# Performance work log

Hardware: AMD Instinct MI355X
Metric: run time of the kernel (lower is better)

Reference implementation:

```python
import jax, jax.numpy as jnp
import numpy as np

UNITS = 50257
CUTOFF = [2000, 10000, UNITS]  # _cutoff = cutoff + [units]
C = 1024                        # channels (d_model)
N = 4096                        # flattened tokens (batch*seq)
N_TAILS = len(CUTOFF) - 1       # 2
ROOT_OUT = CUTOFF[0] + N_TAILS  # 2002
TAIL_DIMS = [256, 64]           # round(C/4**(i+1)/8)*8


def setup_inputs() -> dict:
    key = jax.random.key(0)
    ks = jax.random.split(key, 7)
    logits = jax.random.normal(ks[0], (N, C), jnp.float32)
    targets = jax.random.randint(ks[1], (N,), 0, UNITS, jnp.int32)
    s = 0.02
    head_kernel = jax.random.normal(ks[2], (C, ROOT_OUT), jnp.float32) * s
    proj0 = jax.random.normal(ks[3], (C, TAIL_DIMS[0]), jnp.float32) * s
    scale0 = jax.random.normal(ks[4], (TAIL_DIMS[0], CUTOFF[1] - CUTOFF[0]), jnp.float32) * s
    proj1 = jax.random.normal(ks[5], (C, TAIL_DIMS[1]), jnp.float32) * s
    scale1 = jax.random.normal(ks[6], (TAIL_DIMS[1], CUTOFF[2] - CUTOFF[1]), jnp.float32) * s
    return {"logits": logits, "targets": targets, "head_kernel": head_kernel,
            "proj0": proj0, "scale0": scale0, "proj1": proj1, "scale1": scale1}


def _sparse_ce(lg, labels):
    # sparse softmax cross entropy, numerically stable (single logsumexp)
    lse = jax.nn.logsumexp(lg, axis=-1)
    picked = jnp.take_along_axis(lg, labels[:, None].astype(jnp.int32), axis=1)[:, 0]
    return lse - picked


def reference(logits, targets, head_kernel, proj0, scale0, proj1, scale1):
    # Faithful jax version of AdaptiveSoftmax._train_loss (return_probs=False,
    # dropout=0, no bias on Denses, loss_reduction=SUM_OVER_BATCH_SIZE i.e. mean).
    # Dynamic boolean gather is replaced by dense compute + masked mean, which
    # yields identical math under jit (mean over the routed subset).
    root_logits = (logits @ head_kernel).astype(jnp.float32)  # [N, ROOT_OUT]
    root_targets = targets
    tails = [(proj0, scale0), (proj1, scale1)]
    losses = []
    for i, (p, s) in enumerate(tails):
        lo, hi = CUTOFF[i], CUTOFF[i + 1]
        m = (targets >= lo) & (targets < hi)
        root_targets = jnp.where(m, CUTOFF[0] + i, root_targets)
        tail_logits = ((logits @ p) @ s).astype(jnp.float32)  # [N, hi-lo]
        tail_tgt = jnp.clip(targets - lo, 0, hi - lo - 1)
        ce = _sparse_ce(tail_logits, tail_tgt)
        mf = m.astype(jnp.float32)
        losses.append(jnp.sum(ce * mf) / jnp.maximum(jnp.sum(mf), 1.0))
    root_loss = jnp.mean(_sparse_ce(root_logits, root_targets))
    all_losses = jnp.stack([root_loss] + losses)
    return jnp.mean(all_losses)
```

## Files before the change

### kernel.cpp

```cpp
#include <hip/hip_runtime.h>
#include <math.h>
#include <stdint.h>

#define NROWS 4096
#define CDIM 1024
#define T0_LO 2000
#define T0_HI 10000
#define T1_LO 10000
#define ROOT_COLS 2002
#define ROOT_PAD 2048
#define T0_COLS 8000
#define T0_PAD 8064
#define T1_COLS 40257
#define T1_PAD 40320
#define HB_STRIDE 320
#define LOG2E 1.44269504088896340736f
#define LN2 0.69314718055994530942f

using short8  = __attribute__((ext_vector_type(8))) short;
using ushort8 = __attribute__((ext_vector_type(8))) unsigned short;
using floatx4 = __attribute__((ext_vector_type(4))) float;

__device__ __forceinline__ unsigned short f2bf(float x) {
  union { float f; unsigned int u; } v; v.f = x;
  unsigned int r = v.u + 0x7fffu + ((v.u >> 16) & 1u);
  return (unsigned short)(r >> 16);
}
__device__ __forceinline__ float bf2f(unsigned short h) {
  union { unsigned int u; float f; } v; v.u = ((unsigned int)h) << 16;
  return v.f;
}
__device__ __forceinline__ floatx4 mfma16(short8 a, short8 b, floatx4 c) {
  return __builtin_amdgcn_mfma_f32_16x16x32_bf16(a, b, c, 0, 0, 0);
}
__device__ __forceinline__ void stage16(const unsigned short* g,
                                        unsigned short* lds_wave_base, int lane) {
#if __has_builtin(__builtin_amdgcn_global_load_lds)
  __builtin_amdgcn_global_load_lds(
      (const __attribute__((address_space(1))) void*)g,
      (__attribute__((address_space(3))) void*)lds_wave_base, 16, 0, 0);
#else
  ((ushort8*)lds_wave_base)[lane] = *(const ushort8*)g;
#endif
}

static constexpr size_t B_HB  = 0;
static constexpr size_t B_LB  = B_HB + 4096ull * 320 * 2;
static constexpr size_t B_WP  = B_LB + 4096ull * 1024 * 2;
static constexpr size_t B_WH  = B_WP + 384ull * 1024 * 2;
static constexpr size_t B_WS0 = B_WH + 2048ull * 1024 * 2;
static constexpr size_t B_WS1 = B_WS0 + 8064ull * 256 * 2;
static constexpr size_t B_S   = B_WS1 + 40320ull * 64 * 2;
static constexpr size_t B_P   = B_S + 3ull * 4096 * 4;
static constexpr size_t B_I0  = B_P + 3ull * 4096 * 4;
static constexpr size_t B_I1  = B_I0 + 4096ull * 4;
static constexpr size_t B_CNT = B_I1 + 4096ull * 4;

__device__ __forceinline__ void transpose_tile(
    const float* __restrict__ W, unsigned short* __restrict__ Wt,
    int K, int N, int Npad, int nx, int rel, float scale,
    float (*tile)[33], int tid) {
  const int n0 = (rel % nx) * 32, k0 = (rel / nx) * 32;
  if ((N & 3) == 0) {
    const int lk = tid >> 3, ln = (tid & 7) << 2;
    const int n = n0 + ln;
    float4 v = make_float4(0.f, 0.f, 0.f, 0.f);
    if (n + 3 < N) v = *(const float4*)(W + (size_t)(k0 + lk) * N + n);
    tile[lk][ln]     = v.x * scale;
    tile[lk][ln + 1] = v.y * scale;
    tile[lk][ln + 2] = v.z * scale;
    tile[lk][ln + 3] = v.w * scale;
  } else if ((N & 1) == 0) {
    const int lk = tid >> 4, ln = (tid & 15) << 1;
#pragma unroll
    for (int i = 0; i < 32; i += 16) {
      const int n = n0 + ln;
      float2 v = make_float2(0.f, 0.f);
      if (n + 1 < N) v = *(const float2*)(W + (size_t)(k0 + lk + i) * N + n);
      tile[lk + i][ln]     = v.x * scale;
      tile[lk + i][ln + 1] = v.y * scale;
    }
  } else {
    const int tx = tid & 31, ty = tid >> 5;
    for (int i = 0; i < 32; i += 8) {
      int k = k0 + ty + i, n = n0 + tx;
      tile[ty + i][tx] = (n < N) ? W[(size_t)k * N + n] * scale : 0.f;
    }
  }
  __syncthreads();
  if (tid < 128) {
    const int nloc = tid >> 2, kg = tid & 3;
    const int n = n0 + nloc;
    if (n < Npad) {
      ushort8 x;
#pragma unroll
      for (int j = 0; j < 8; j++) x[j] = f2bf(tile[kg * 8 + j][nloc]);
      *(ushort8*)&Wt[(size_t)n * K + k0 + kg * 8] = x;
    }
  }
}

#define PP_WH_END   2048
#define PP_WS0_END  (PP_WH_END + 2016)
#define PP_WS1_END  (PP_WS0_END + 2520)
#define PP_WP0_END  (PP_WS1_END + 256)
#define PP_WP1_END  (PP_WP0_END + 64)
#define PP_LB_END   (PP_WP1_END + 2048)
#define PP_ZERO_END (PP_LB_END + 32)
#define PP_S_END    (PP_ZERO_END + 4)
#define PP_TOTAL    (PP_S_END + 1)

__global__ __launch_bounds__(256) void prep_kernel(
    const float* __restrict__ head, const float* __restrict__ proj0,
    const float* __restrict__ proj1, const float* __restrict__ scale0,
    const float* __restrict__ scale1, const float* __restrict__ logits,
    const int* __restrict__ targets,
    unsigned short* __restrict__ Wh, unsigned short* __restrict__ Wp,
    unsigned short* __restrict__ Ws0, unsigned short* __restrict__ Ws1,
    unsigned short* __restrict__ Lb, float* __restrict__ S,
    int* __restrict__ idx0, int* __restrict__ idx1, int* __restrict__ cnt) {
  __shared__ float tile[32][33];
  const int id = blockIdx.x, tid = threadIdx.x;
  if (id < PP_WP1_END) {
    const float* W; unsigned short* Wt; int K, N, Npad, nx, rel; float scale;
    if (id < PP_WH_END)        { W = head;   Wt = Wh;  K = 1024; N = ROOT_COLS; Npad = ROOT_PAD; scale = LOG2E; nx = 64;   rel = id; }
    else if (id < PP_WS0_END)  { W = scale0; Wt = Ws0; K = 256;  N = T0_COLS;   Npad = T0_PAD;   scale = LOG2E; nx = 252;  rel = id - PP_WH_END; }
    else if (id < PP_WS1_END)  { W = scale1; Wt = Ws1; K = 64;   N = T1_COLS;   Npad = T1_PAD;   scale = LOG2E; nx = 1260; rel = id - PP_WS0_END; }
    else if (id < PP_WP0_END)  { W = proj0;  Wt = Wp;  K = 1024; N = 256;       Npad = 256;      scale = 1.f;   nx = 8;    rel = id - PP_WS1_END; }
    else                       { W = proj1;  Wt = Wp + 256 * 1024; K = 1024; N = 64; Npad = 64; scale = 1.f; nx = 2; rel = id - PP_WP0_END; }
    transpose_tile(W, Wt, K, N, Npad, nx, rel, scale, tile, tid);
    return;
  }
  if (id < PP_LB_END) {
    size_t base = (size_t)(id - PP_WP1_END) * 2048 + tid * 8;
    float4 v0 = *(const float4*)(logits + base);
    float4 v1 = *(const float4*)(logits + base + 4);
    ushort8 h;
    h[0] = f2bf(v0.x); h[1] = f2bf(v0.y); h[2] = f2bf(v0.z); h[3] = f2bf(v0.w);
    h[4] = f2bf(v1.x); h[5] = f2bf(v1.y); h[6] = f2bf(v1.z); h[7] = f2bf(v1.w);
    *(ushort8*)(Lb + base) = h;
    return;
  }
  if (id < PP_ZERO_END) {
    size_t off = (size_t)(id - PP_LB_END) * 2048 + tid * 8;
    ushort8 z = {0, 0, 0, 0, 0, 0, 0, 0};
    *(ushort8*)(Wp + 320ull * 1024 + off) = z;
    return;
  }
  if (id < PP_S_END) {
    int rel = id - PP_ZERO_END;
    float4 z = make_float4(0.f, 0.f, 0.f, 0.f);
#pragma unroll
    for (int j = 0; j < 3; j++)
      ((float4*)S)[rel * 768 + j * 256 + tid] = z;
    return;
  }
  __shared__ int base2[2];
  if (tid < 2) base2[tid] = 0;
  __syncthreads();
  for (int n = tid; n < NROWS; n += 256) {
    int t = targets[n];
    if (t >= T0_LO && t < T0_HI) idx0[atomicAdd(&base2[0], 1)] = n;
    else if (t >= T1_LO)         idx1[atomicAdd(&base2[1], 1)] = n;
  }
  __syncthreads();
  if (tid < 2) cnt[tid] = base2[tid];
}

template<int CI>
__device__ __forceinline__ void gemm64_kloop(
    unsigned short* A_lds,
    const unsigned short* Arow,
    const unsigned short* const (&Bbase)[CI],
    floatx4 (&acc)[CI][4], int tid) {
  const int lane = tid & 63, w = tid >> 6;
  const int m = lane & 15, quad = lane >> 4, keym = m & 7;
  int goff[4];
#pragma unroll
  for (int it = 0; it < 4; it++) {
    int s = w * 256 + it * 64 + lane;
    int r = s >> 4, p = s & 15;
    int cq = p ^ (r & 7);
    goff[it] = r * CDIM + cq * 8;
  }
#pragma unroll
  for (int it = 0; it < 4; it++)
    stage16(Arow + goff[it], &A_lds[(w * 256 + it * 64) * 8], lane);
  for (int h = 0; h < 8; h++) {
    unsigned short* cur = A_lds + (h & 1) * (64 * 128);
    unsigned short* nxt = A_lds + ((h + 1) & 1) * (64 * 128);
    __syncthreads();
    if (h + 1 < 8) {
#pragma unroll
      for (int it = 0; it < 4; it++)
        stage16(Arow + goff[it] + (h + 1) * 128,
                &nxt[(w * 256 + it * 64) * 8], lane);
    }
    short8 b[CI][4];
#pragma unroll
    for (int ci = 0; ci < CI; ci++)
#pragma unroll
      for (int ks = 0; ks < 4; ks++)
        b[ci][ks] = *(const short8*)(Bbase[ci] + h * 128 + ks * 32);
    short8 areg[4][4];
#pragma unroll
    for (int t = 0; t < 4; t++)
#pragma unroll
      for (int ks = 0; ks < 4; ks++) {
        int ch = ((ks << 2) + quad) ^ keym;
        areg[t][ks] = *(const short8*)&cur[(t * 16 + m) * 128 + (ch << 3)];
      }
#pragma unroll
    for (int ci = 0; ci < CI; ci++)
#pragma unroll
      for (int ks = 0; ks < 4; ks++)
#pragma unroll
        for (int t = 0; t < 4; t++)
          acc[ci][t] = mfma16(areg[t][ks], b[ci][ks], acc[ci][t]);
  }
}

__global__ __launch_bounds__(256) void hidden_kernel(
    const unsigned short* __restrict__ Lb,
    const unsigned short* __restrict__ Wp,
    unsigned short* __restrict__ Hb) {
  __shared__ unsigned short A_lds[64 * 256];
  const int id = blockIdx.x, tid = threadIdx.x;
  const int xcd = id & 7, k = id >> 3;
  const int row0 = (xcd * 8 + (k & 7)) * 64;
  const int cg0 = k >> 3;
  const int lane = tid & 63, w = tid >> 6;
  const int m = lane & 15, quad = lane >> 4;
  const floatx4 zf = {0.f, 0.f, 0.f, 0.f};
  floatx4 acc[1][4];
#pragma unroll
  for (int t = 0; t < 4; t++) acc[0][t] = zf;
  const unsigned short* Bb[1] = {
      Wp + (size_t)(cg0 * 64 + w * 16 + m) * CDIM + quad * 8};
  gemm64_kloop<1>(A_lds, Lb + (size_t)row0 * CDIM, Bb, acc, tid);
  int n = cg0 * 64 + w * 16 + m;
  if (n < HB_STRIDE) {
#pragma unroll
    for (int t = 0; t < 4; t++)
#pragma unroll
      for (int r = 0; r < 4; r++)
        Hb[(size_t)(row0 + t * 16 + quad * 4 + r) * HB_STRIDE + n] =
            f2bf(acc[0][t][r]);
  }
}

#define MG_ROOT 512
#define MG_T1   480
#define MG_T0   2688
#define MG_PICK 1024
#define MG_TOTAL (MG_ROOT + MG_T1 + MG_T0 + MG_PICK)

__device__ __forceinline__ void root_compute(
    const unsigned short* cur, const short8 (&b)[2][2], floatx4 (&acc)[2][8],
    int m, int quad, int keym) {
#pragma unroll
  for (int hf = 0; hf < 2; hf++) {
    short8 areg[4][2];
#pragma unroll
    for (int t = 0; t < 4; t++)
#pragma unroll
      for (int ks = 0; ks < 2; ks++) {
        int ch = ((ks << 2) + quad) ^ keym;
        areg[t][ks] = *(const short8*)&cur[(hf * 64 + t * 16 + m) * 64 + (ch << 3)];
      }
#pragma unroll
    for (int ci = 0; ci < 2; ci++)
#pragma unroll
      for (int ks = 0; ks < 2; ks++)
#pragma unroll
        for (int t = 0; t < 4; t++)
          acc[ci][hf * 4 + t] = mfma16(areg[t][ks], b[ci][ks], acc[ci][hf * 4 + t]);
  }
}

__device__ __forceinline__ void root_stage(
    const unsigned short* Arow, const int (&goff)[4], int koff,
    unsigned short* buf, int w, int lane) {
#pragma unroll
  for (int it = 0; it < 4; it++)
    stage16(Arow + goff[it] + koff, &buf[(it * 256 + w * 64) * 8], lane);
}

__device__ __forceinline__ void root_loadB(
    const unsigned short* const (&Bb)[2], int koff, short8 (&b)[2][2]) {
#pragma unroll
  for (int ci = 0; ci < 2; ci++)
#pragma unroll
    for (int ks = 0; ks < 2; ks++)
      b[ci][ks] = *(const short8*)(Bb[ci] + koff + ks * 32);
}

__device__ __forceinline__ void root_path(
    unsigned char* smem, int bx, int by,
    const unsigned short* __restrict__ Lb,
    const unsigned short* __restrict__ Wh, float* __restrict__ S) {
  unsigned short* bufA = (unsigned short*)smem;
  unsigned short* bufB = bufA + 128 * 64;
  const int tid = threadIdx.x;
  const int row0 = bx * 128;
  const int cg0 = by * 2;
  const int lane = tid & 63, w = tid >> 6;
  const int m = lane & 15, quad = lane >> 4, keym = m & 7;
  const floatx4 zf = {0.f, 0.f, 0.f, 0.f};
  floatx4 acc[2][8];
#pragma unroll
  for (int ci = 0; ci < 2; ci++)
#pragma unroll
    for (int t = 0; t < 8; t++) acc[ci][t] = zf;
  const unsigned short* Bb[2] = {
      Wh + (size_t)((cg0 + 0) * 64 + w * 16 + m) * CDIM + quad * 8,
      Wh + (size_t)((cg0 + 1) * 64 + w * 16 + m) * CDIM + quad * 8};
  const unsigned short* Arow = Lb + (size_t)row0 * CDIM;
  int goff[4];
#pragma unroll
  for (int it = 0; it < 4; it++) {
    int s = it * 256 + w * 64 + lane;
    int r = s >> 3, p = s & 7;
    int cq = p ^ (r & 7);
    goff[it] = r * CDIM + cq * 8;
  }
  short8 b0[2][2], b1[2][2];
  root_stage(Arow, goff, 0, bufA, w, lane);
  root_loadB(Bb, 0, b0);
  for (int hh = 0; hh < 8; hh++) {
    __syncthreads();
    root_stage(Arow, goff, (hh * 2 + 1) * 64, bufB, w, lane);
    root_loadB(Bb, (hh * 2 + 1) * 64, b1);
    root_compute(bufA, b0, acc, m, quad, keym);
    __syncthreads();
    if (hh < 7) {
      root_stage(Arow, goff, (hh * 2 + 2) * 64, bufA, w, lane);
      root_loadB(Bb, (hh * 2 + 2) * 64, b0);
    }
    root_compute(bufB, b1, acc, m, quad, keym);
  }
  __syncthreads();
  float* sums = (float*)smem;
  if (tid < 128) sums[tid] = 0.f;
  __syncthreads();
#pragma unroll
  for (int t = 0; t < 8; t++)
#pragma unroll
    for (int r = 0; r < 4; r++) {
      float e = __builtin_amdgcn_exp2f(acc[0][t][r]) +
                __builtin_amdgcn_exp2f(acc[1][t][r]);
      e += __shfl_xor(e, 1); e += __shfl_xor(e, 2);
      e += __shfl_xor(e, 4); e += __shfl_xor(e, 8);
      if (m == 0)
        atomicAdd(&sums[(t >> 2) * 64 + (t & 3) * 16 + quad * 4 + r], e);
    }
  __syncthreads();
  if (tid < 128) atomicAdd(&S[row0 + tid], sums[tid]);
}

template<int K, int TILES, int MODE>
__device__ __forceinline__ void tail_path(
    unsigned char* smem, int bx, int by,
    const unsigned short* __restrict__ Hb, int acol0,
    const unsigned short* __restrict__ Wt, int ncgpb,
    const int* __restrict__ idx, const int* __restrict__ cnt,
    float* __restrict__ S) {
  constexpr int BM = TILES * 16;
  constexpr int CpR = K / 8;
  constexpr int KS = K / 32;
  unsigned short* A_lds = (unsigned short*)smem;
  int* row_lds = (int*)(smem + (size_t)BM * K * 2);
  float* sum_lds = (float*)(smem + (size_t)BM * K * 2 + BM * 4);
  const int tid = threadIdx.x;
  const int count = cnt[MODE - 1];
  const int row0 = bx * BM;
  if (row0 >= count) return;
  if (tid < BM) {
    int r = row0 + tid;
    row_lds[tid] = (r < count) ? idx[r] : -1;
    sum_lds[tid] = 0.f;
  }
  __syncthreads();
#pragma unroll
  for (int i = 0; i < BM * CpR / 256; i++) {
    int c = tid + 256 * i;
    int rl = c / CpR, cq = c % CpR;
    int row = row_lds[rl];
    ushort8 v = {0, 0, 0, 0, 0, 0, 0, 0};
    if (row >= 0) v = *(const ushort8*)(Hb + (size_t)row * HB_STRIDE + acol0 + cq * 8);
    *(ushort8*)&A_lds[rl * K + ((cq ^ (rl & 7)) << 3)] = v;
  }
  __syncthreads();
  const int lane = tid & 63, w = tid >> 6;
  const int m = lane & 15, quad = lane >> 4, keym = m & 7;
  const floatx4 zf = {0.f, 0.f, 0.f, 0.f};
  short8 areg[TILES][KS];
#pragma unroll
  for (int t = 0; t < TILES; t++)
#pragma unroll
    for (int ks = 0; ks < KS; ks++) {
      int ch = ((ks << 2) + quad) ^ keym;
      areg[t][ks] = *(const short8*)&A_lds[(t * 16 + m) * K + (ch << 3)];
    }
  float runsum[TILES][4];
#pragma unroll
  for (int t = 0; t < TILES; t++)
#pragma unroll
    for (int r = 0; r < 4; r++) runsum[t][r] = 0.f;

  const int cg0 = by * ncgpb;
  const unsigned short* Bp = Wt + (size_t)(cg0 * 64 + w * 16 + m) * K + quad * 8;
  short8 b0[KS], b1[KS];
#pragma unroll
  for (int ks = 0; ks < KS; ks++) b0[ks] = *(const short8*)(Bp + ks * 32);
#pragma unroll
  for (int ks = 0; ks < KS; ks++)
    b1[ks] = *(const short8*)(Bp + (size_t)64 * K + ks * 32);

  for (int cc = 0; cc < ncgpb; cc += 2) {
    floatx4 acc[TILES];
#pragma unroll
    for (int t = 0; t < TILES; t++) acc[t] = zf;
#pragma unroll
    for (int ks = 0; ks < KS; ks++)
#pragma unroll
      for (int t = 0; t < TILES; t++) acc[t] = mfma16(areg[t][ks], b0[ks], acc[t]);
    if (cc + 2 < ncgpb) {
      const unsigned short* p = Bp + (size_t)(cc + 2) * 64 * K;
#pragma unroll
      for (int ks = 0; ks < KS; ks++) b0[ks] = *(const short8*)(p + ks * 32);
    }
#pragma unroll
    for (int t = 0; t < TILES; t++)
#pragma unroll
      for (int r = 0; r < 4; r++)
        runsum[t][r] += __builtin_amdgcn_exp2f(acc[t][r]);

#pragma unroll
    for (int t = 0; t < TILES; t++) acc[t] = zf;
#pragma unroll
    for (int ks = 0; ks < KS; ks++)
#pragma unroll
      for (int t = 0; t < TILES; t++) acc[t] = mfma16(areg[t][ks], b1[ks], acc[t]);
    if (cc + 3 < ncgpb) {
      const unsigned short* p = Bp + (size_t)(cc + 3) * 64 * K;
#pragma unroll
      for (int ks = 0; ks < KS; ks++) b1[ks] = *(const short8*)(p + ks * 32);
    }
#pragma unroll
    for (int t = 0; t < TILES; t++)
#pragma unroll
      for (int r = 0; r < 4; r++)
        runsum[t][r] += __builtin_amdgcn_exp2f(acc[t][r]);
  }

#pragma unroll
  for (int t = 0; t < TILES; t++)
#pragma unroll
    for (int r = 0; r < 4; r++) {
      float e = runsum[t][r];
      e += __shfl_xor(e, 1); e += __shfl_xor(e, 2);
      e += __shfl_xor(e, 4); e += __shfl_xor(e, 8);
      if (m == 0) atomicAdd(&sum_lds[t * 16 + quad * 4 + r], e);
    }
  __syncthreads();
  if (tid < BM) {
    int row = row_lds[tid];
    if (row >= 0) atomicAdd(&S[row], sum_lds[tid]);
  }
}

__device__ __forceinline__ void picked_path(
    int rel, const float* __restrict__ logits, const int* __restrict__ targets,
    const unsigned short* __restrict__ Wh,
    const unsigned short* __restrict__ Ws0,
    const unsigned short* __restrict__ Ws1,
    const unsigned short* __restrict__ Hb, float* __restrict__ P) {
  const int tid = threadIdx.x, lane = tid & 63;
  const int row = rel * 4 + (tid >> 6);
  const int t = targets[row];
  const int tr = (t >= T0_LO && t < T0_HI) ? T0_LO : ((t >= T1_LO) ? T0_LO + 1 : t);
  const float* a = logits + (size_t)row * CDIM + lane * 16;
  const unsigned short* wr = Wh + (size_t)tr * CDIM + lane * 16;
  float acc = 0.f;
#pragma unroll
  for (int q = 0; q < 2; q++) {
    ushort8 wv = *(const ushort8*)(wr + q * 8);
    float4 a0 = ((const float4*)a)[q * 2];
    float4 a1 = ((const float4*)a)[q * 2 + 1];
    acc += a0.x * bf2f(wv[0]) + a0.y * bf2f(wv[1]) + a0.z * bf2f(wv[2]) + a0.w * bf2f(wv[3]);
    acc += a1.x * bf2f(wv[4]) + a1.y * bf2f(wv[5]) + a1.z * bf2f(wv[6]) + a1.w * bf2f(wv[7]);
  }
#pragma unroll
  for (int off = 1; off < 64; off <<= 1) acc += __shfl_xor(acc, off);
  if (lane == 0) P[row] = acc * LN2;
  if (t >= T0_LO) {
    float acc2 = 0.f;
    if (t < T0_HI) {
      const unsigned short* h = Hb + (size_t)row * HB_STRIDE + lane * 4;
      const unsigned short* w2 = Ws0 + (size_t)(t - T0_LO) * 256 + lane * 4;
#pragma unroll
      for (int j = 0; j < 4; j++) acc2 += bf2f(h[j]) * bf2f(w2[j]);
    } else {
      acc2 = bf2f(Hb[(size_t)row * HB_STRIDE + 256 + lane]) *
             bf2f(Ws1[(size_t)(t - T1_LO) * 64 + lane]);
    }
#pragma unroll
    for (int off = 1; off < 64; off <<= 1) acc2 += __shfl_xor(acc2, off);
    if (lane == 0) P[(t < T0_HI ? NROWS : 2 * NROWS) + row] = acc2 * LN2;
  }
}

__global__ __launch_bounds__(256, 2) void mega_kernel(
    const unsigned short* __restrict__ Lb,
    const unsigned short* __restrict__ Wh,
    const unsigned short* __restrict__ Ws0,
    const unsigned short* __restrict__ Ws1,
    const unsigned short* __restrict__ Hb,
    const float* __restrict__ logits, const int* __restrict__ targets,
    const int* __restrict__ idx0, const int* __restrict__ idx1,
    const int* __restrict__ cnt, float* __restrict__ S, float* __restrict__ P) {
  __shared__ __align__(16) unsigned char smem[32768];
  int bid = blockIdx.x;
  if (bid < MG_ROOT) {
    int wk = ((bid & 7) << 6) + (bid >> 3);
    root_path(smem, wk >> 4, wk & 15, Lb, Wh, S);
    return;
  }
  bid -= MG_ROOT;
  if (bid < MG_T1) {
    int wk = (bid & 7) * 60 + (bid >> 3);
    tail_path<64, 8, 2>(smem, wk & 31, wk >> 5, Hb, 256, Ws1, 42, idx1, cnt,
                        S + 2 * NROWS);
    return;
  }
  bid -= MG_T1;
  if (bid < MG_T0) {
    int wk = (bid & 7) * 336 + (bid >> 3);
    tail_path<256, 2, 1>(smem, wk & 127, wk >> 7, Hb, 0, Ws0, 6, idx0, cnt,
                         S + NROWS);
    return;
  }
  bid -= MG_T0;
  picked_path(bid, logits, targets, Wh, Ws0, Ws1, Hb, P);
}

__global__ __launch_bounds__(1024) void loss_kernel(
    const int* __restrict__ targets,
    const float* __restrict__ S,
    const float* __restrict__ P,
    float* __restrict__ out) {
  const int tid = threadIdx.x;
  float sr = 0.f, s0 = 0.f, s1 = 0.f, c0 = 0.f, c1 = 0.f;
  for (int n = tid; n < NROWS; n += 1024) {
    int t = targets[n];
    sr += logf(S[n] - 46.f) - P[n];
    if (t >= T0_LO && t < T0_HI) { s0 += logf(S[NROWS + n] - 64.f) - P[NROWS + n]; c0 += 1.f; }
    else if (t >= T1_LO)         { s1 += logf(S[2 * NROWS + n] - 63.f) - P[2 * NROWS + n]; c1 += 1.f; }
  }
  for (int off = 32; off > 0; off >>= 1) {
    sr += __shfl_down(sr, off);
    s0 += __shfl_down(s0, off);
    s1 += __shfl_down(s1, off);
    c0 += __shfl_down(c0, off);
    c1 += __shfl_down(c1, off);
  }
  __shared__ float red[16][5];
  int wv = tid >> 6;
  if ((tid & 63) == 0) { red[wv][0] = sr; red[wv][1] = s0; red[wv][2] = s1; red[wv][3] = c0; red[wv][4] = c1; }
  __syncthreads();
  if (tid == 0) {
    sr = 0.f; s0 = 0.f; s1 = 0.f; c0 = 0.f; c1 = 0.f;
#pragma unroll
    for (int i = 0; i < 16; i++) {
      sr += red[i][0]; s0 += red[i][1]; s1 += red[i][2];
      c0 += red[i][3]; c1 += red[i][4];
    }
    float root_loss = sr / (float)NROWS;
    float l0 = s0 / fmaxf(c0, 1.f);
    float l1 = s1 / fmaxf(c1, 1.f);
    out[0] = (root_loss + l0 + l1) / 3.f;
  }
}

extern "C" void kernel_launch(void* const* d_in, const int* in_sizes, int n_in,
                              void* d_out, int out_size, void* d_ws, size_t ws_size,
                              hipStream_t stream) {
  const float* logits  = (const float*)d_in[0];
  const int*   targets = (const int*)d_in[1];
  const float* head    = (const float*)d_in[2];
  const float* proj0   = (const float*)d_in[3];
  const float* scale0  = (const float*)d_in[4];
  const float* proj1   = (const float*)d_in[5];
  const float* scale1  = (const float*)d_in[6];
  float* out = (float*)d_out;
  char* ws = (char*)d_ws;

  unsigned short* Hb  = (unsigned short*)(ws + B_HB);
  unsigned short* Lb  = (unsigned short*)(ws + B_LB);
  unsigned short* Wp  = (unsigned short*)(ws + B_WP);
  unsigned short* Wh  = (unsigned short*)(ws + B_WH);
  unsigned short* Ws0 = (unsigned short*)(ws + B_WS0);
  unsigned short* Ws1 = (unsigned short*)(ws + B_WS1);
  float* S = (float*)(ws + B_S);
  float* P = (float*)(ws + B_P);
  int* idx0 = (int*)(ws + B_I0);
  int* idx1 = (int*)(ws + B_I1);
  int* cnt  = (int*)(ws + B_CNT);

  prep_kernel<<<PP_TOTAL, 256, 0, stream>>>(head, proj0, proj1, scale0, scale1,
                                            logits, targets, Wh, Wp, Ws0, Ws1,
                                            Lb, S, idx0, idx1, cnt);
  hidden_kernel<<<320, 256, 0, stream>>>(Lb, Wp, Hb);
  mega_kernel<<<MG_TOTAL, 256, 0, stream>>>(Lb, Wh, Ws0, Ws1, Hb, logits,
                                            targets, idx0, idx1, cnt, S, P);
  loss_kernel<<<1, 1024, 0, stream>>>(targets, S, P, out);
}
```

Baseline: 185.2 us.

## Fuse four kernel launches into one cooperative persistent kernel with grid syncs

Merges the prep, hidden, mega and loss kernels into a single cooperative kernel of 512 blocks. Each block loops over the virtual block indices of every stage, with grid-wide syncs separating the stages. The aim is to remove the launch gaps and tail idle time between kernels. The trade-off is a fixed grid of 512 at 2 blocks per CU, which may lower occupancy, the cost of the grid barriers, and the 32 KB shared allocation now applying to prep too. If the cooperative launch fails, it falls back to the separate kernels.

```diff
diff --git a/kernel.cpp b/kernel.cpp
--- a/kernel.cpp
+++ b/kernel.cpp
@@ -1,6 +1,9 @@
 #include <hip/hip_runtime.h>
+#include <hip/hip_cooperative_groups.h>
 #include <math.h>
 #include <stdint.h>
+
+namespace cg = cooperative_groups;
 
 #define NROWS 4096
 #define CDIM 1024
@@ -16,6 +19,7 @@
 #define HB_STRIDE 320
 #define LOG2E 1.44269504088896340736f
 #define LN2 0.69314718055994530942f
+#define GRID 512
 
 using short8  = __attribute__((ext_vector_type(8))) short;
 using ushort8 = __attribute__((ext_vector_type(8))) unsigned short;
@@ -110,7 +114,8 @@
 #define PP_S_END    (PP_ZERO_END + 4)
 #define PP_TOTAL    (PP_S_END + 1)
 
-__global__ __launch_bounds__(256) void prep_kernel(
+__device__ __forceinline__ void prep_block(
+    int id, int tid, unsigned char* smem,
     const float* __restrict__ head, const float* __restrict__ proj0,
     const float* __restrict__ proj1, const float* __restrict__ scale0,
     const float* __restrict__ scale1, const float* __restrict__ logits,
@@ -119,8 +124,7 @@
     unsigned short* __restrict__ Ws0, unsigned short* __restrict__ Ws1,
     unsigned short* __restrict__ Lb, float* __restrict__ S,
     int* __restrict__ idx0, int* __restrict__ idx1, int* __restrict__ cnt) {
-  __shared__ float tile[32][33];
-  const int id = blockIdx.x, tid = threadIdx.x;
+  float (*tile)[33] = (float(*)[33])smem;
   if (id < PP_WP1_END) {
     const float* W; unsigned short* Wt; int K, N, Npad, nx, rel; float scale;
     if (id < PP_WH_END)        { W = head;   Wt = Wh;  K = 1024; N = ROOT_COLS; Npad = ROOT_PAD; scale = LOG2E; nx = 64;   rel = id; }
@@ -155,7 +159,7 @@
       ((float4*)S)[rel * 768 + j * 256 + tid] = z;
     return;
   }
-  __shared__ int base2[2];
+  int* base2 = (int*)smem;
   if (tid < 2) base2[tid] = 0;
   __syncthreads();
   for (int n = tid; n < NROWS; n += 256) {
@@ -220,12 +224,12 @@
   }
 }
 
-__global__ __launch_bounds__(256) void hidden_kernel(
+__device__ __forceinline__ void hidden_block(
+    int id, int tid, unsigned char* smem,
     const unsigned short* __restrict__ Lb,
     const unsigned short* __restrict__ Wp,
     unsigned short* __restrict__ Hb) {
-  __shared__ unsigned short A_lds[64 * 256];
-  const int id = blockIdx.x, tid = threadIdx.x;
+  unsigned short* A_lds = (unsigned short*)smem;
   const int xcd = id & 7, k = id >> 3;
   const int row0 = (xcd * 8 + (k & 7)) * 64;
   const int cg0 = k >> 3;
@@ -511,7 +515,141 @@
   }
 }
 
-__global__ __launch_bounds__(256, 2) void mega_kernel(
+__device__ __forceinline__ void mega_block(
+    int bid, unsigned char* smem,
+    const unsigned short* __restrict__ Lb,
+    const unsigned short* __restrict__ Wh,
+    const unsigned short* __restrict__ Ws0,
+    const unsigned short* __restrict__ Ws1,
+    const unsigned short* __restrict__ Hb,
+    const float* __restrict__ logits, const int* __restrict__ targets,
+    const int* __restrict__ idx0, const int* __restrict__ idx1,
+    const int* __restrict__ cnt, float* __restrict__ S, float* __restrict__ P) {
+  if (bid < MG_ROOT) {
+    int wk = ((bid & 7) << 6) + (bid >> 3);
+    root_path(smem, wk >> 4, wk & 15, Lb, Wh, S);
+    return;
+  }
+  bid -= MG_ROOT;
+  if (bid < MG_T1) {
+    int wk = (bid & 7) * 60 + (bid >> 3);
+    tail_path<64, 8, 2>(smem, wk & 31, wk >> 5, Hb, 256, Ws1, 42, idx1, cnt,
+                        S + 2 * NROWS);
+    return;
+  }
+  bid -= MG_T1;
+  if (bid < MG_T0) {
+    int wk = (bid & 7) * 336 + (bid >> 3);
+    tail_path<256, 2, 1>(smem, wk & 127, wk >> 7, Hb, 0, Ws0, 6, idx0, cnt,
+                         S + NROWS);
+    return;
+  }
+  bid -= MG_T0;
+  picked_path(bid, logits, targets, Wh, Ws0, Ws1, Hb, P);
+}
+
+__device__ __forceinline__ void loss_block(
+    int tid, unsigned char* smem, const int* __restrict__ targets,
+    const float* __restrict__ S, const float* __restrict__ P,
+    float* __restrict__ out) {
+  float sr = 0.f, s0 = 0.f, s1 = 0.f, c0 = 0.f, c1 = 0.f;
+  for (int n = tid; n < NROWS; n += 256) {
+    int t = targets[n];
+    sr += logf(S[n] - 46.f) - P[n];
+    if (t >= T0_LO && t < T0_HI) { s0 += logf(S[NROWS + n] - 64.f) - P[NROWS + n]; c0 += 1.f; }
+    else if (t >= T1_LO)         { s1 += logf(S[2 * NROWS + n] - 63.f) - P[2 * NROWS + n]; c1 += 1.f; }
+  }
+  for (int off = 32; off > 0; off >>= 1) {
+    sr += __shfl_down(sr, off);
+    s0 += __shfl_down(s0, off);
+    s1 += __shfl_down(s1, off);
+    c0 += __shfl_down(c0, off);
+    c1 += __shfl_down(c1, off);
+  }
+  float (*red)[5] = (float(*)[5])smem;
+  int wv = tid >> 6;
+  if ((tid & 63) == 0) { red[wv][0] = sr; red[wv][1] = s0; red[wv][2] = s1; red[wv][3] = c0; red[wv][4] = c1; }
+  __syncthreads();
+  if (tid == 0) {
+    sr = 0.f; s0 = 0.f; s1 = 0.f; c0 = 0.f; c1 = 0.f;
+#pragma unroll
+    for (int i = 0; i < 4; i++) {
+      sr += red[i][0]; s0 += red[i][1]; s1 += red[i][2];
+      c0 += red[i][3]; c1 += red[i][4];
+    }
+    float root_loss = sr / (float)NROWS;
+    float l0 = s0 / fmaxf(c0, 1.f);
+    float l1 = s1 / fmaxf(c1, 1.f);
+    out[0] = (root_loss + l0 + l1) / 3.f;
+  }
+}
+
+__global__ __launch_bounds__(256, 2) void uber_kernel(
+    const float* __restrict__ logits, const int* __restrict__ targets,
+    const float* __restrict__ head, const float* __restrict__ proj0,
+    const float* __restrict__ scale0, const float* __restrict__ proj1,
+    const float* __restrict__ scale1, char* __restrict__ ws,
+    float* __restrict__ out) {
+  __shared__ __align__(16) unsigned char smem[32768];
+  unsigned short* Hb  = (unsigned short*)(ws + B_HB);
+  unsigned short* Lb  = (unsigned short*)(ws + B_LB);
+  unsigned short* Wp  = (unsigned short*)(ws + B_WP);
+  unsigned short* Wh  = (unsigned short*)(ws + B_WH);
+  unsigned short* Ws0 = (unsigned short*)(ws + B_WS0);
+  unsigned short* Ws1 = (unsigned short*)(ws + B_WS1);
+  float* S = (float*)(ws + B_S);
+  float* P = (float*)(ws + B_P);
+  int* idx0 = (int*)(ws + B_I0);
+  int* idx1 = (int*)(ws + B_I1);
+  int* cnt  = (int*)(ws + B_CNT);
+  const int bid = blockIdx.x, tid = threadIdx.x;
+
+  for (int vb = bid; vb < PP_TOTAL; vb += GRID) {
+    prep_block(vb, tid, smem, head, proj0, proj1, scale0, scale1, logits,
+               targets, Wh, Wp, Ws0, Ws1, Lb, S, idx0, idx1, cnt);
+    __syncthreads();
+  }
+  __threadfence();
+  cg::this_grid().sync();
+
+  for (int vb = bid; vb < 320; vb += GRID)
+    hidden_block(vb, tid, smem, Lb, Wp, Hb);
+  __threadfence();
+  cg::this_grid().sync();
+
+  for (int vb = bid; vb < MG_TOTAL; vb += GRID) {
+    mega_block(vb, smem, Lb, Wh, Ws0, Ws1, Hb, logits, targets, idx0, idx1,
+               cnt, S, P);
+    __syncthreads();
+  }
+  __threadfence();
+  cg::this_grid().sync();
+
+  if (bid == 0) loss_block(tid, smem, targets, S, P, out);
+}
+
+__global__ __launch_bounds__(256) void prep_kernel_g(
+    const float* __restrict__ head, const float* __restrict__ proj0,
+    const float* __restrict__ proj1, const float* __restrict__ scale0,
+    const float* __restrict__ scale1, const float* __restrict__ logits,
+    const int* __restrict__ targets,
+    unsigned short* __restrict__ Wh, unsigned short* __restrict__ Wp,
+    unsigned short* __restrict__ Ws0, unsigned short* __restrict__ Ws1,
+    unsigned short* __restrict__ Lb, float* __restrict__ S,
+    int* __restrict__ idx0, int* __restrict__ idx1, int* __restrict__ cnt) {
+  __shared__ __align__(16) unsigned char smem[4352];
+  prep_block(blockIdx.x, threadIdx.x, smem, head, proj0, proj1, scale0, scale1,
+             logits, targets, Wh, Wp, Ws0, Ws1, Lb, S, idx0, idx1, cnt);
+}
+
+__global__ __launch_bounds__(256) void hidden_kernel_g(
+    const unsigned short* __restrict__ Lb, const unsigned short* __restrict__ Wp,
+    unsigned short* __restrict__ Hb) {
+  __shared__ __align__(16) unsigned char smem[32768];
+  hidden_block(blockIdx.x, threadIdx.x, smem, Lb, Wp, Hb);
+}
+
+__global__ __launch_bounds__(256, 2) void mega_kernel_g(
     const unsigned short* __restrict__ Lb,
     const unsigned short* __restrict__ Wh,
     const unsigned short* __restrict__ Ws0,
@@ -521,66 +659,15 @@
     const int* __restrict__ idx0, const int* __restrict__ idx1,
     const int* __restrict__ cnt, float* __restrict__ S, float* __restrict__ P) {
   __shared__ __align__(16) unsigned char smem[32768];
-  int bid = blockIdx.x;
-  if (bid < MG_ROOT) {
-    int wk = ((bid & 7) << 6) + (bid >> 3);
-    root_path(smem, wk >> 4, wk & 15, Lb, Wh, S);
-    return;
-  }
-  bid -= MG_ROOT;
-  if (bid < MG_T1) {
-    int wk = (bid & 7) * 60 + (bid >> 3);
-    tail_path<64, 8, 2>(smem, wk & 31, wk >> 5, Hb, 256, Ws1, 42, idx1, cnt,
-                        S + 2 * NROWS);
-    return;
-  }
-  bid -= MG_T1;
-  if (bid < MG_T0) {
-    int wk = (bid & 7) * 336 + (bid >> 3);
-    tail_path<256, 2, 1>(smem, wk & 127, wk >> 7, Hb, 0, Ws0, 6, idx0, cnt,
-                         S + NROWS);
-    return;
-  }
-  bid -= MG_T0;
-  picked_path(bid, logits, targets, Wh, Ws0, Ws1, Hb, P);
-}
-
-__global__ __launch_bounds__(1024) void loss_kernel(
-    const int* __restrict__ targets,
-    const float* __restrict__ S,
-    const float* __restrict__ P,
-    float* __restrict__ out) {
-  const int tid = threadIdx.x;
-  float sr = 0.f, s0 = 0.f, s1 = 0.f, c0 = 0.f, c1 = 0.f;
-  for (int n = tid; n < NROWS; n += 1024) {
-    int t = targets[n];
-    sr += logf(S[n] - 46.f) - P[n];
-    if (t >= T0_LO && t < T0_HI) { s0 += logf(S[NROWS + n] - 64.f) - P[NROWS + n]; c0 += 1.f; }
-    else if (t >= T1_LO)         { s1 += logf(S[2 * NROWS + n] - 63.f) - P[2 * NROWS + n]; c1 += 1.f; }
-  }
-  for (int off = 32; off > 0; off >>= 1) {
-    sr += __shfl_down(sr, off);
-    s0 += __shfl_down(s0, off);
-    s1 += __shfl_down(s1, off);
-    c0 += __shfl_down(c0, off);
-    c1 += __shfl_down(c1, off);
-  }
-  __shared__ float red[16][5];
-  int wv = tid >> 6;
-  if ((tid & 63) == 0) { red[wv][0] = sr; red[wv][1] = s0; red[wv][2] = s1; red[wv][3] = c0; red[wv][4] = c1; }
-  __syncthreads();
-  if (tid == 0) {
-    sr = 0.f; s0 = 0.f; s1 = 0.f; c0 = 0.f; c1 = 0.f;
-#pragma unroll
-    for (int i = 0; i < 16; i++) {
-      sr += red[i][0]; s0 += red[i][1]; s1 += red[i][2];
-      c0 += red[i][3]; c1 += red[i][4];
-    }
-    float root_loss = sr / (float)NROWS;
-    float l0 = s0 / fmaxf(c0, 1.f);
-    float l1 = s1 / fmaxf(c1, 1.f);
-    out[0] = (root_loss + l0 + l1) / 3.f;
-  }
+  mega_block(blockIdx.x, smem, Lb, Wh, Ws0, Ws1, Hb, logits, targets, idx0,
+             idx1, cnt, S, P);
+}
+
+__global__ __launch_bounds__(256) void loss_kernel_g(
+    const int* __restrict__ targets, const float* __restrict__ S,
+    const float* __restrict__ P, float* __restrict__ out) {
+  __shared__ __align__(16) unsigned char smem[128];
+  loss_block(threadIdx.x, smem, targets, S, P, out);
 }
 
 extern "C" void kernel_launch(void* const* d_in, const int* in_sizes, int n_in,
@@ -596,6 +683,13 @@
   float* out = (float*)d_out;
   char* ws = (char*)d_ws;
 
+  void* args[] = {(void*)&logits, (void*)&targets, (void*)&head, (void*)&proj0,
+                  (void*)&scale0, (void*)&proj1, (void*)&scale1, (void*)&ws,
+                  (void*)&out};
+  hipError_t err = hipLaunchCooperativeKernel(
+      (const void*)uber_kernel, dim3(GRID), dim3(256), args, 0, stream);
+  if (err == hipSuccess) return;
+
   unsigned short* Hb  = (unsigned short*)(ws + B_HB);
   unsigned short* Lb  = (unsigned short*)(ws + B_LB);
   unsigned short* Wp  = (unsigned short*)(ws + B_WP);
@@ -607,12 +701,11 @@
   int* idx0 = (int*)(ws + B_I0);
   int* idx1 = (int*)(ws + B_I1);
   int* cnt  = (int*)(ws + B_CNT);
-
-  prep_kernel<<<PP_TOTAL, 256, 0, stream>>>(head, proj0, proj1, scale0, scale1,
-                                            logits, targets, Wh, Wp, Ws0, Ws1,
-                                            Lb, S, idx0, idx1, cnt);
-  hidden_kernel<<<320, 256, 0, stream>>>(Lb, Wp, Hb);
-  mega_kernel<<<MG_TOTAL, 256, 0, stream>>>(Lb, Wh, Ws0, Ws1, Hb, logits,
-                                            targets, idx0, idx1, cnt, S, P);
-  loss_kernel<<<1, 1024, 0, stream>>>(targets, S, P, out);
-}
+  prep_kernel_g<<<PP_TOTAL, 256, 0, stream>>>(head, proj0, proj1, scale0,
+                                              scale1, logits, targets, Wh, Wp,
+                                              Ws0, Ws1, Lb, S, idx0, idx1, cnt);
+  hidden_kernel_g<<<320, 256, 0, stream>>>(Lb, Wp, Hb);
+  mega_kernel_g<<<MG_TOTAL, 256, 0, stream>>>(Lb, Wh, Ws0, Ws1, Hb, logits,
+                                              targets, idx0, idx1, cnt, S, P);
+  loss_kernel_g<<<1, 256, 0, stream>>>(targets, S, P, out);
+}
```

Measured after the change: 557.8 us. 201% more time.
